# Optimization experiments

Hardware: AMD Instinct MI355X
Metric: run time of the kernel (lower is better)

The kernel has to match this reference:

```python
import jax, jax.numpy as jnp
import numpy as np

B, IN = 8192, 8000
C, S, O = 16, 500, 64          # num_chunks, chunk_size, fc_repr_dim
F = C * O                       # fc_0_out_feat = 1024
E, D, T = 8, 512, 2            # num_experts, fc_task_dim, num_tasks
NC = (32, 2)                    # num_classes per task
EPS = 1e-5


def _bn(h, g, b, axis):
    # training-mode BatchNorm1d: biased variance over the batch axis
    m = h.mean(axis=axis, keepdims=True)
    v = h.var(axis=axis, keepdims=True)
    return (h - m) * jax.lax.rsqrt(v + EPS) * g + b


def _swish(x):
    return x * jax.nn.sigmoid(x)


def setup_inputs() -> dict:
    key = jax.random.key(0)
    ks = jax.random.split(key, 10)
    s = 0.02
    return {
        "x": jax.random.normal(ks[0], (B, IN), dtype=jnp.float32),
        "w0": jax.random.normal(ks[1], (C, O, S), dtype=jnp.float32) * s,
        "b0": jnp.zeros((F,), jnp.float32),
        "bn0_g": jnp.ones((F,), jnp.float32),
        "bn0_b": jnp.zeros((F,), jnp.float32),
        "gate_w": jax.random.normal(ks[2], (T, F, E), dtype=jnp.float32) * s,
        "gate_b": jnp.zeros((T, E), jnp.float32),
        "exp_w": jax.random.normal(ks[3], (E, F, D), dtype=jnp.float32) * s,
        "exp_bn_g": jnp.ones((E, D), jnp.float32),
        "exp_bn_b": jnp.zeros((E, D), jnp.float32),
        "task_w": jax.random.normal(ks[4], (T, D, D), dtype=jnp.float32) * s,
        "task_bn_g": jnp.ones((T, D), jnp.float32),
        "task_bn_b": jnp.zeros((T, D), jnp.float32),
        "fin_w_a": jax.random.normal(ks[5], (D, NC[0]), dtype=jnp.float32) * s,
        "fin_b_a": jnp.zeros((NC[0],), jnp.float32),
        "fin_w_b": jax.random.normal(ks[6], (D, NC[1]), dtype=jnp.float32) * s,
        "fin_b_b": jnp.zeros((NC[1],), jnp.float32),
    }


def reference(x, w0, b0, bn0_g, bn0_b, gate_w, gate_b, exp_w, exp_bn_g,
              exp_bn_b, task_w, task_bn_g, task_bn_b, fin_w_a, fin_b_a,
              fin_w_b, fin_b_b):
    b = x.shape[0]
    # SplitLinear: block-diagonal linear over C chunks of size S -> O each
    h0 = jnp.einsum('bcs,cos->bco', x.reshape(b, C, S), w0).reshape(b, F) + b0
    h0 = _swish(_bn(h0, bn0_g, bn0_b, axis=0))                  # [B, F]
    # per-task gates with softmax over experts
    gates = jax.nn.softmax(
        jnp.einsum('bf,tfe->tbe', h0, gate_w) + gate_b[:, None, :], axis=-1)
    # expert branches: Linear(no bias) + BN + Swish, vectorized over experts
    eh = jnp.einsum('bf,efd->bed', h0, exp_w)                   # [B, E, D]
    eh = _swish(_bn(eh, exp_bn_g, exp_bn_b, axis=0))
    # gate-weighted sum over experts, per task
    mix = jnp.einsum('tbe,bed->tbd', gates, eh)                 # [T, B, D]
    # task branches: Linear(no bias) + BN + Swish
    th = jnp.einsum('tbd,tdk->tbk', mix, task_w)
    th = _swish(_bn(th, task_bn_g[:, None, :], task_bn_b[:, None, :], axis=1))
    out_a = th[0] @ fin_w_a + fin_b_a                           # [B, 32]
    out_b = th[1] @ fin_w_b + fin_b_b                           # [B, 2]
    return jnp.concatenate([out_a, out_b], axis=1)             # [B, 34]
```

## Files before the change

kernel.cpp:

```cpp
#include <hip/hip_runtime.h>
#include <math.h>

#define B_ 8192
#define IN_ 8000
#define C_ 16
#define S_ 500
#define O_ 64
#define F_ 1024
#define E_ 8
#define D_ 512
#define T_ 2
#define OUTW 34
#define EPS_ 1e-5f

typedef __attribute__((ext_vector_type(8))) short bf16x8;
typedef __attribute__((ext_vector_type(4))) float f32x4;

__device__ __forceinline__ float swishf(float x) {
    return x / (1.0f + __expf(-x));
}

__device__ __forceinline__ unsigned short f2bf(float f) {
    union { float f; unsigned u; } c;
    c.f = f;
    unsigned r = c.u + 0x7fffu + ((c.u >> 16) & 1u);
    return (unsigned short)(r >> 16);
}
__device__ __forceinline__ float bf2f(unsigned short b) {
    union { unsigned u; float f; } c;
    c.u = ((unsigned)b) << 16;
    return c.f;
}

__device__ __forceinline__ void gld16(const void* g, void* l) {
    __builtin_amdgcn_global_load_lds(
        (const __attribute__((address_space(1))) void*)g,
        (__attribute__((address_space(3))) void*)l, 16, 0, 0);
}

__global__ __launch_bounds__(256) void k_split(const float* __restrict__ x,
                                               const float* __restrict__ w0,
                                               const float* __restrict__ b0,
                                               unsigned short* __restrict__ h0raw,
                                               float* __restrict__ psum,
                                               float* __restrict__ psq) {
    __shared__ __align__(16) unsigned short As[128 * 72];
    __shared__ __align__(16) unsigned short Bs[64 * 72];
    int tid = threadIdx.x;
    int c = blockIdx.y;
    int brow0 = blockIdx.x * 128;
    const float* xp = x + (size_t)brow0 * IN_ + c * S_;
    const float* wp = w0 + (size_t)c * O_ * S_;

    int w = tid >> 6, lane = tid & 63;
    int l15 = lane & 15, quad = lane >> 4;
    int wm = w * 32;

    f32x4 acc[2][4] = {};

    for (int k0 = 0; k0 < 512; k0 += 64) {
#pragma unroll
        for (int i = 0; i < 8; i++) {
            int li = tid + i * 256;
            int row = li >> 4, c4 = li & 15;
            int gk = k0 + c4 * 4;
            float4 v = make_float4(0.f, 0.f, 0.f, 0.f);
            if (gk + 3 < S_) v = *(const float4*)(xp + (size_t)row * IN_ + gk);
            unsigned short u[4] = { f2bf(v.x), f2bf(v.y), f2bf(v.z), f2bf(v.w) };
            *(ushort4*)&As[row * 72 + c4 * 4] = *(ushort4*)u;
        }
#pragma unroll
        for (int i = 0; i < 4; i++) {
            int li = tid + i * 256;
            int row = li >> 4, c4 = li & 15;
            int gk = k0 + c4 * 4;
            float4 v = make_float4(0.f, 0.f, 0.f, 0.f);
            if (gk + 3 < S_) v = *(const float4*)(wp + (size_t)row * S_ + gk);
            unsigned short u[4] = { f2bf(v.x), f2bf(v.y), f2bf(v.z), f2bf(v.w) };
            *(ushort4*)&Bs[row * 72 + c4 * 4] = *(ushort4*)u;
        }
        __syncthreads();
#pragma unroll
        for (int kk = 0; kk < 64; kk += 32) {
            bf16x8 af[2], wf[4];
#pragma unroll
            for (int i = 0; i < 2; i++)
                af[i] = *(const bf16x8*)&As[(wm + i * 16 + l15) * 72 + kk + quad * 8];
#pragma unroll
            for (int j = 0; j < 4; j++)
                wf[j] = *(const bf16x8*)&Bs[(j * 16 + l15) * 72 + kk + quad * 8];
#pragma unroll
            for (int i = 0; i < 2; i++)
#pragma unroll
                for (int j = 0; j < 4; j++)
                    acc[i][j] = __builtin_amdgcn_mfma_f32_16x16x32_bf16(af[i], wf[j], acc[i][j], 0, 0, 0);
        }
        __syncthreads();
    }

    int colbase = c * O_;
    float sj[4], qj[4];
#pragma unroll
    for (int j = 0; j < 4; j++) {
        int col = j * 16 + l15;
        float bb = b0[colbase + col];
        float s = 0.f, q = 0.f;
#pragma unroll
        for (int i = 0; i < 2; i++) {
#pragma unroll
            for (int reg = 0; reg < 4; reg++) {
                float v = acc[i][j][reg] + bb;
                int rl = wm + i * 16 + quad * 4 + reg;
                h0raw[(size_t)(brow0 + rl) * F_ + colbase + col] = f2bf(v);
                s += v; q += v * v;
            }
        }
        s += __shfl_down(s, 32, 64); s += __shfl_down(s, 16, 64);
        q += __shfl_down(q, 32, 64); q += __shfl_down(q, 16, 64);
        sj[j] = s; qj[j] = q;
    }
    __syncthreads();
    float* red = (float*)As;
    if (lane < 16) {
#pragma unroll
        for (int j = 0; j < 4; j++) {
            int col = j * 16 + l15;
            red[col * 4 + w] = sj[j];
            red[256 + col * 4 + w] = qj[j];
        }
    }
    __syncthreads();
    if (tid < 64) {
        float ss = red[tid * 4] + red[tid * 4 + 1] + red[tid * 4 + 2] + red[tid * 4 + 3];
        float qq = red[256 + tid * 4] + red[256 + tid * 4 + 1] + red[256 + tid * 4 + 2] + red[256 + tid * 4 + 3];
        size_t idx = (size_t)blockIdx.x * F_ + colbase + tid;
        psum[idx] = ss; psq[idx] = qq;
    }
}

__global__ __launch_bounds__(64) void k_stats_b(const float* __restrict__ psum,
                                                const float* __restrict__ psq,
                                                int N, int YS,
                                                const float* __restrict__ g,
                                                const float* __restrict__ beta,
                                                unsigned long long gslab,
                                                float* __restrict__ scale,
                                                float* __restrict__ shift,
                                                unsigned long long oslab) {
    int n = blockIdx.x * 64 + threadIdx.x;
    int z = blockIdx.z;
    float s = 0.f, q = 0.f;
    for (int y = 0; y < YS; y++) {
        size_t idx = ((size_t)(z * YS + y)) * N + n;
        s += psum[idx]; q += psq[idx];
    }
    float mean = s * (1.0f / B_);
    float var = q * (1.0f / B_) - mean * mean;
    float sc = g[z * gslab + n] * rsqrtf(var + EPS_);
    scale[z * oslab + n] = sc;
    shift[z * oslab + n] = beta[z * gslab + n] - mean * sc;
}

__global__ __launch_bounds__(256) void k_wt(const float* __restrict__ in,
                                            unsigned short* __restrict__ out,
                                            int K, int N) {
    __shared__ float t[32][33];
    int k0 = blockIdx.x * 32, n0 = blockIdx.y * 32, z = blockIdx.z;
    const float* ip = in + (size_t)z * K * N;
    unsigned short* op = out + (size_t)z * N * K;
    int tn = threadIdx.x & 31, tk = threadIdx.x >> 5;
#pragma unroll
    for (int p = 0; p < 4; p++) {
        int k = tk + p * 8;
        t[k][tn] = ip[(size_t)(k0 + k) * N + n0 + tn];
    }
    __syncthreads();
    int tk2 = threadIdx.x & 31, tn2 = threadIdx.x >> 5;
#pragma unroll
    for (int p = 0; p < 4; p++) {
        int n = tn2 + p * 8;
        op[(size_t)(n0 + n) * K + k0 + tk2] = f2bf(t[tk2][n]);
    }
}

__global__ __launch_bounds__(256) void k_bnswish_gates(const unsigned short* __restrict__ h0,
                                                       const float* __restrict__ scale,
                                                       const float* __restrict__ shift,
                                                       const float* __restrict__ gate_w,
                                                       const float* __restrict__ gate_b,
                                                       unsigned short* __restrict__ h0bf,
                                                       float* __restrict__ gates) {
    int b = blockIdx.x, tid = threadIdx.x;
    float part[16];
#pragma unroll
    for (int i = 0; i < 16; i++) part[i] = 0.f;
    const unsigned short* row = h0 + (size_t)b * F_;
    unsigned short* ob = h0bf + (size_t)b * F_;
    int f0 = tid * 4;
    ushort4 u = *(const ushort4*)(row + f0);
    float4 sc4 = *(const float4*)(scale + f0);
    float4 sh4 = *(const float4*)(shift + f0);
    unsigned short uu[4] = { u.x, u.y, u.z, u.w };
    float scv[4] = { sc4.x, sc4.y, sc4.z, sc4.w };
    float shv[4] = { sh4.x, sh4.y, sh4.z, sh4.w };
    unsigned short ov[4];
#pragma unroll
    for (int j = 0; j < 4; j++) {
        float sw = swishf(scv[j] * bf2f(uu[j]) + shv[j]);
        ov[j] = f2bf(sw);
        const float* gw0 = gate_w + (size_t)(f0 + j) * E_;
        const float* gw1 = gw0 + (size_t)F_ * E_;
#pragma unroll
        for (int e = 0; e < E_; e++) part[e] += sw * gw0[e];
#pragma unroll
        for (int e = 0; e < E_; e++) part[8 + e] += sw * gw1[e];
    }
    *(ushort4*)(ob + f0) = *(ushort4*)ov;
#pragma unroll
    for (int i = 0; i < 16; i++) {
        float v = part[i];
        for (int off = 32; off > 0; off >>= 1) v += __shfl_down(v, off, 64);
        part[i] = v;
    }
    __shared__ float red[4][16];
    __shared__ float gfin[16];
    int wave = tid >> 6, lane = tid & 63;
    if (lane == 0) {
#pragma unroll
        for (int i = 0; i < 16; i++) red[wave][i] = part[i];
    }
    __syncthreads();
    if (tid < 16) {
        float v = red[0][tid] + red[1][tid] + red[2][tid] + red[3][tid];
        int t = tid >> 3, e = tid & 7;
        gfin[tid] = v + gate_b[t * E_ + e];
    }
    __syncthreads();
    if (tid < 2) {
        float mx = -1e30f;
#pragma unroll
        for (int e = 0; e < 8; e++) mx = fmaxf(mx, gfin[tid * 8 + e]);
        float ex[8], sum = 0.f;
#pragma unroll
        for (int e = 0; e < 8; e++) { ex[e] = __expf(gfin[tid * 8 + e] - mx); sum += ex[e]; }
        float inv = 1.0f / sum;
#pragma unroll
        for (int e = 0; e < 8; e++)
            gates[(size_t)tid * (B_ * E_) + (size_t)b * E_ + e] = ex[e] * inv;
    }
}

__global__ __launch_bounds__(256) void k_gemm_bf16(const unsigned short* __restrict__ A,
                                                   unsigned long long aslab,
                                                   const unsigned short* __restrict__ Wt,
                                                   unsigned long long wslab,
                                                   unsigned short* __restrict__ C,
                                                   unsigned long long cslab, int K,
                                                   float* __restrict__ psum,
                                                   float* __restrict__ psq) {
    __shared__ __align__(16) unsigned short As[128 * 32];
    __shared__ __align__(16) unsigned short Ws[128 * 32];
    int z = blockIdx.z;
    A  += (size_t)z * aslab;
    Wt += (size_t)z * wslab;
    C  += (size_t)z * cslab;
    const int N = gridDim.y * 128;
    int row0 = blockIdx.x * 128, col0 = blockIdx.y * 128;
    int tid = threadIdx.x;
    int w = tid >> 6, lane = tid & 63;
    int l15 = lane & 15, quad = lane >> 4;

    const unsigned short* ga0 = A  + (size_t)(row0 + w * 32 + (lane >> 2)) * K + (lane & 3) * 8;
    const unsigned short* ga1 = ga0 + 16 * (size_t)K;
    const unsigned short* gw0 = Wt + (size_t)(col0 + w * 32 + (lane >> 2)) * K + (lane & 3) * 8;
    const unsigned short* gw1 = gw0 + 16 * (size_t)K;
    unsigned short* la0 = As + (w * 32) * 32;
    unsigned short* la1 = As + (w * 32 + 16) * 32;
    unsigned short* lw0 = Ws + (w * 32) * 32;
    unsigned short* lw1 = Ws + (w * 32 + 16) * 32;

    int wm = (w & 1) * 64, wn = (w >> 1) * 64;
    const unsigned short* Afr = As + (size_t)(wm + l15) * 32 + quad * 8;
    const unsigned short* Wfr = Ws + (size_t)(wn + l15) * 32 + quad * 8;

    f32x4 acc[4][4] = {};

    for (int k0 = 0; k0 < K; k0 += 32) {
        gld16(ga0 + k0, la0);
        gld16(ga1 + k0, la1);
        gld16(gw0 + k0, lw0);
        gld16(gw1 + k0, lw1);
        __syncthreads();
        bf16x8 af[4], wf[4];
#pragma unroll
        for (int i = 0; i < 4; i++) af[i] = *(const bf16x8*)(Afr + i * 16 * 32);
#pragma unroll
        for (int j = 0; j < 4; j++) wf[j] = *(const bf16x8*)(Wfr + j * 16 * 32);
#pragma unroll
        for (int i = 0; i < 4; i++)
#pragma unroll
            for (int j = 0; j < 4; j++)
                acc[i][j] = __builtin_amdgcn_mfma_f32_16x16x32_bf16(af[i], wf[j], acc[i][j], 0, 0, 0);
        __syncthreads();
    }

#pragma unroll
    for (int i = 0; i < 4; i++) {
        int r = row0 + wm + i * 16 + quad * 4;
#pragma unroll
        for (int j = 0; j < 4; j++) {
            int cc = col0 + wn + j * 16 + l15;
            unsigned short* cp = C + (size_t)r * N + cc;
#pragma unroll
            for (int reg = 0; reg < 4; reg++)
                cp[(size_t)reg * N] = f2bf(acc[i][j][reg]);
        }
    }

    float* red = (float*)As;
    float sj[4], qj[4];
#pragma unroll
    for (int j = 0; j < 4; j++) {
        float s = 0.f, q = 0.f;
#pragma unroll
        for (int i = 0; i < 4; i++)
#pragma unroll
            for (int reg = 0; reg < 4; reg++) {
                float v = acc[i][j][reg];
                s += v; q += v * v;
            }
        s += __shfl_down(s, 32, 64); s += __shfl_down(s, 16, 64);
        q += __shfl_down(q, 32, 64); q += __shfl_down(q, 16, 64);
        sj[j] = s; qj[j] = q;
    }
    if (lane < 16) {
#pragma unroll
        for (int j = 0; j < 4; j++) {
            int cib = wn + j * 16 + lane;
            red[cib * 2 + (w & 1)] = sj[j];
            red[256 + cib * 2 + (w & 1)] = qj[j];
        }
    }
    __syncthreads();
    if (tid < 128) {
        float s = red[tid * 2] + red[tid * 2 + 1];
        float q = red[256 + tid * 2] + red[256 + tid * 2 + 1];
        size_t row = (size_t)z * gridDim.x + blockIdx.x;
        psum[row * N + col0 + tid] = s;
        psq[row * N + col0 + tid] = q;
    }
}

__global__ __launch_bounds__(512, 2) void k_gemm256(const unsigned short* __restrict__ A,
                                                    const unsigned short* __restrict__ Wt,
                                                    unsigned short* __restrict__ Cc,
                                                    int N, int K,
                                                    float* __restrict__ psum,
                                                    float* __restrict__ psq) {
    __shared__ __align__(16) unsigned short lds[2][2][2][8192];
    int tid = threadIdx.x;
    int w = tid >> 6, lane = tid & 63;
    int l15 = lane & 15, quad = lane >> 4;
    int wm = w >> 2, wn = w & 3;

    int lin = blockIdx.y * gridDim.x + blockIdx.x;
    int cpx = (gridDim.x * gridDim.y) >> 3;
    int swz = (lin & 7) * cpx + (lin >> 3);
    int bx = swz & (gridDim.x - 1), by = swz / gridDim.x;
    int row0 = bx * 256, col0 = by * 256;

    int srow = tid >> 3, sperm = (tid & 7) ^ (srow & 7);
    const unsigned short* pA = A  + (size_t)(row0 + srow) * K + sperm * 8;
    const unsigned short* pB = Wt + (size_t)(col0 + srow) * K + sperm * 8;

    int aoffs[2];
#pragma unroll
    for (int kk = 0; kk < 2; kk++)
        aoffs[kk] = l15 * 64 + ((kk * 4 + quad) ^ (l15 & 7)) * 8;

    f32x4 acc[8][4] = {};
    bf16x8 afr[4][2], bfr[2][2];
    int nt = K >> 6;

#define STAGE256(t1, nb) do {                                                              \
    const unsigned short* sA = pA + (size_t)(t1) * 64;                                     \
    const unsigned short* sB = pB + (size_t)(t1) * 64;                                     \
    _Pragma("unroll")                                                                      \
    for (int h = 0; h < 2; h++)                                                            \
        _Pragma("unroll")                                                                  \
        for (int L = 0; L < 2; L++) {                                                      \
            gld16(sA + (size_t)(h * 128 + L * 64) * K, &lds[nb][0][h][w * 512 + L * 4096]);\
            gld16(sB + (size_t)(h * 128 + L * 64) * K, &lds[nb][1][h][w * 512 + L * 4096]);\
        }                                                                                  \
} while (0)

#define LDA256(mh) do {                                                                    \
    _Pragma("unroll")                                                                      \
    for (int mf = 0; mf < 4; mf++)                                                         \
        _Pragma("unroll")                                                                  \
        for (int kk = 0; kk < 2; kk++)                                                     \
            afr[mf][kk] = *(const bf16x8*)(Ab + ((mh) * 4 + mf) * 1024 + aoffs[kk]);       \
} while (0)

#define LDB256(nh) do {                                                                    \
    _Pragma("unroll")                                                                      \
    for (int nf = 0; nf < 2; nf++)                                                         \
        _Pragma("unroll")                                                                  \
        for (int kk = 0; kk < 2; kk++)                                                     \
            bfr[nf][kk] = *(const bf16x8*)(Bb + ((nh) * 2 + nf) * 1024 + aoffs[kk]);       \
} while (0)

#define MMA256(mh, nh) do {                                                                \
    _Pragma("unroll")                                                                      \
    for (int mf = 0; mf < 4; mf++)                                                         \
        _Pragma("unroll")                                                                  \
        for (int nf = 0; nf < 2; nf++)                                                     \
            _Pragma("unroll")                                                              \
            for (int kk = 0; kk < 2; kk++)                                                 \
                acc[(mh) * 4 + mf][(nh) * 2 + nf] = __builtin_amdgcn_mfma_f32_16x16x32_bf16(\
                    afr[mf][kk], bfr[nf][kk], acc[(mh) * 4 + mf][(nh) * 2 + nf], 0, 0, 0); \
} while (0)

#define PHASE_MID()                                                                        \
    __builtin_amdgcn_s_barrier();                                                          \
    asm volatile("s_waitcnt lgkmcnt(0)" ::: "memory");                                     \
    __builtin_amdgcn_sched_barrier(0);                                                     \
    __builtin_amdgcn_s_setprio(1);

#define PHASE_END()                                                                        \
    __builtin_amdgcn_s_setprio(0);                                                         \
    __builtin_amdgcn_sched_barrier(0);                                                     \
    __builtin_amdgcn_s_barrier();

    STAGE256(0, 0);
    asm volatile("s_waitcnt vmcnt(0)" ::: "memory");
    __builtin_amdgcn_s_barrier();

    for (int t = 0; t < nt; t++) {
        int buf = t & 1;
        const unsigned short* Ab = &lds[buf][0][wm][0];
        const unsigned short* Bb = &lds[buf][1][wn >> 1][(wn & 1) * 4096];
        LDA256(0); LDB256(0);
        if (t + 1 < nt) STAGE256(t + 1, buf ^ 1);
        PHASE_MID();
        MMA256(0, 0);
        PHASE_END();
        LDB256(1);
        PHASE_MID();
        MMA256(0, 1);
        PHASE_END();
        LDA256(1);
        PHASE_MID();
        MMA256(1, 1);
        PHASE_END();
        LDB256(0);
        PHASE_MID();
        MMA256(1, 0);
        __builtin_amdgcn_s_setprio(0);
        __builtin_amdgcn_sched_barrier(0);
        asm volatile("s_waitcnt vmcnt(0)" ::: "memory");
        __builtin_amdgcn_s_barrier();
    }
#undef STAGE256
#undef LDA256
#undef LDB256
#undef MMA256
#undef PHASE_MID
#undef PHASE_END

    __syncthreads();

#pragma unroll
    for (int mf = 0; mf < 8; mf++) {
        int r = row0 + wm * 128 + mf * 16 + quad * 4;
#pragma unroll
        for (int nf = 0; nf < 4; nf++) {
            int cc = col0 + wn * 64 + nf * 16 + l15;
            unsigned short* cp = Cc + (size_t)r * N + cc;
#pragma unroll
            for (int reg = 0; reg < 4; reg++)
                cp[(size_t)reg * N] = f2bf(acc[mf][nf][reg]);
        }
    }

    float* red = (float*)&lds[0][0][0][0];
    float* redq = red + 512;
    float sj[4], qj[4];
#pragma unroll
    for (int nf = 0; nf < 4; nf++) {
        float s = 0.f, q = 0.f;
#pragma unroll
        for (int mf = 0; mf < 8; mf++)
#pragma unroll
            for (int reg = 0; reg < 4; reg++) {
                float v = acc[mf][nf][reg];
                s += v; q += v * v;
            }
        s += __shfl_down(s, 32, 64); s += __shfl_down(s, 16, 64);
        q += __shfl_down(q, 32, 64); q += __shfl_down(q, 16, 64);
        sj[nf] = s; qj[nf] = q;
    }
    if (quad == 0) {
#pragma unroll
        for (int nf = 0; nf < 4; nf++) {
            int cib = wn * 64 + nf * 16 + l15;
            red[cib * 2 + wm] = sj[nf];
            redq[cib * 2 + wm] = qj[nf];
        }
    }
    __syncthreads();
    if (tid < 256) {
        float s = red[tid * 2] + red[tid * 2 + 1];
        float q = redq[tid * 2] + redq[tid * 2 + 1];
        psum[(size_t)bx * N + col0 + tid] = s;
        psq [(size_t)bx * N + col0 + tid] = q;
    }
}

__global__ __launch_bounds__(256) void k_mix(const unsigned short* __restrict__ eh,
                                             const float* __restrict__ scale,
                                             const float* __restrict__ shift,
                                             const float* __restrict__ gates,
                                             unsigned short* __restrict__ mix) {
    __shared__ float scl[E_ * D_], shl[E_ * D_];
    __shared__ float gl[2][2][8];
    int tid = threadIdx.x;
#pragma unroll
    for (int i = 0; i < 4; i++) {
        int li = tid + i * 256;
        ((float4*)scl)[li] = ((const float4*)scale)[li];
        ((float4*)shl)[li] = ((const float4*)shift)[li];
    }
    if (tid < 32) {
        int sub = tid >> 4, t = (tid >> 3) & 1, e = tid & 7;
        gl[sub][t][e] = gates[(size_t)t * (B_ * E_) + (size_t)(blockIdx.x * 2 + sub) * E_ + e];
    }
    __syncthreads();
    int sub = tid >> 7;
    int b = blockIdx.x * 2 + sub;
    int d0 = (tid & 127) * 4;
    float a0[4] = {0.f, 0.f, 0.f, 0.f}, a1[4] = {0.f, 0.f, 0.f, 0.f};
#pragma unroll
    for (int e = 0; e < E_; e++) {
        ushort4 u = *(const ushort4*)&eh[(size_t)b * (E_ * D_) + e * D_ + d0];
        float4 sc4 = *(const float4*)&scl[e * D_ + d0];
        float4 sh4 = *(const float4*)&shl[e * D_ + d0];
        float g0 = gl[sub][0][e], g1 = gl[sub][1][e];
        unsigned short uu[4] = { u.x, u.y, u.z, u.w };
        float scv[4] = { sc4.x, sc4.y, sc4.z, sc4.w };
        float shv[4] = { sh4.x, sh4.y, sh4.z, sh4.w };
#pragma unroll
        for (int l = 0; l < 4; l++) {
            float sw = swishf(scv[l] * bf2f(uu[l]) + shv[l]);
            a0[l] += g0 * sw;
            a1[l] += g1 * sw;
        }
    }
    unsigned short o0[4], o1[4];
#pragma unroll
    for (int l = 0; l < 4; l++) { o0[l] = f2bf(a0[l]); o1[l] = f2bf(a1[l]); }
    *(ushort4*)&mix[(size_t)b * D_ + d0] = *(ushort4*)o0;
    *(ushort4*)&mix[(size_t)(B_ * D_) + (size_t)b * D_ + d0] = *(ushort4*)o1;
}

__global__ __launch_bounds__(256) void k_final(const unsigned short* __restrict__ th,
                                               const float* __restrict__ scale,
                                               const float* __restrict__ shift,
                                               const float* __restrict__ fwa,
                                               const float* __restrict__ fba,
                                               const float* __restrict__ fwb,
                                               const float* __restrict__ fbb,
                                               float* __restrict__ out) {
    __shared__ float t0[8][D_], t1[8][D_];
    __shared__ float pb[64];
    int tid = threadIdx.x;
    int b0 = blockIdx.x * 8;
#pragma unroll
    for (int t = 0; t < 2; t++) {
#pragma unroll
        for (int i = 0; i < 4; i++) {
            int li = tid + i * 256;
            int row = li >> 7, d = (li & 127) * 4;
            ushort4 u = *(const ushort4*)&th[((size_t)t * B_ + b0 + row) * D_ + d];
            unsigned short uu[4] = { u.x, u.y, u.z, u.w };
            float* dst = t ? &t1[row][d] : &t0[row][d];
#pragma unroll
            for (int l = 0; l < 4; l++)
                dst[l] = swishf(scale[t * D_ + d + l] * bf2f(uu[l]) + shift[t * D_ + d + l]);
        }
    }
    __syncthreads();
    {
        int row = tid >> 5, col = tid & 31;
        float acc = fba[col];
        for (int d = 0; d < D_; d++) acc += t0[row][d] * fwa[d * 32 + col];
        out[(size_t)(b0 + row) * OUTW + col] = acc;
    }
    if (tid < 64) {
        int row = tid >> 3, colb = (tid >> 2) & 1, part = tid & 3;
        float a = 0.f;
        for (int d = part * 128; d < part * 128 + 128; d++) a += t1[row][d] * fwb[d * 2 + colb];
        pb[tid] = a;
    }
    __syncthreads();
    if (tid < 16) {
        int row = tid >> 1, colb = tid & 1;
        int base = row * 8 + colb * 4;
        float a = fbb[colb] + pb[base] + pb[base + 1] + pb[base + 2] + pb[base + 3];
        out[(size_t)(b0 + row) * OUTW + 32 + colb] = a;
    }
}

extern "C" void kernel_launch(void* const* d_in, const int* in_sizes, int n_in,
                              void* d_out, int out_size, void* d_ws, size_t ws_size,
                              hipStream_t stream) {
    const float* x        = (const float*)d_in[0];
    const float* w0       = (const float*)d_in[1];
    const float* b0       = (const float*)d_in[2];
    const float* bn0_g    = (const float*)d_in[3];
    const float* bn0_b    = (const float*)d_in[4];
    const float* gate_w   = (const float*)d_in[5];
    const float* gate_b   = (const float*)d_in[6];
    const float* exp_w    = (const float*)d_in[7];
    const float* exp_bn_g = (const float*)d_in[8];
    const float* exp_bn_b = (const float*)d_in[9];
    const float* task_w   = (const float*)d_in[10];
    const float* task_bn_g= (const float*)d_in[11];
    const float* task_bn_b= (const float*)d_in[12];
    const float* fwa      = (const float*)d_in[13];
    const float* fba      = (const float*)d_in[14];
    const float* fwb      = (const float*)d_in[15];
    const float* fbb      = (const float*)d_in[16];
    float* out = (float*)d_out;

    float* ws = (float*)d_ws;
    unsigned short* ehbf  = (unsigned short*)ws;
    unsigned short* h0raw = (unsigned short*)(ws + 16777216);
    unsigned short* thbf  = ehbf;
    unsigned short* mixbf = h0raw;
    unsigned short* h0bf  = (unsigned short*)(ws + 20971520);
    unsigned short* wtE   = (unsigned short*)(ws + 25165824);
    unsigned short* twt   = (unsigned short*)(ws + 27262976);
    float* gates = ws + 27525120;
    float* sc0   = ws + 27656192;
    float* sh0   = sc0 + 1024;
    float* scE   = sh0 + 1024;
    float* shE   = scE + 4096;
    float* scT   = shE + 4096;
    float* shT   = scT + 1024;
    float* psum  = shT + 1024;
    float* psq   = psum + 262144;

    k_wt<<<dim3(32, 16, 8), 256, 0, stream>>>(exp_w, wtE, F_, D_);
    k_wt<<<dim3(16, 16, 2), 256, 0, stream>>>(task_w, twt, D_, D_);
    k_split<<<dim3(64, 16), 256, 0, stream>>>(x, w0, b0, h0raw, psum, psq);
    k_stats_b<<<dim3(16, 1, 1), 64, 0, stream>>>(psum, psq, F_, 64, bn0_g, bn0_b, 0ull, sc0, sh0, 0ull);
    k_bnswish_gates<<<dim3(B_), 256, 0, stream>>>(h0raw, sc0, sh0, gate_w, gate_b, h0bf, gates);
    k_gemm256<<<dim3(32, 16), 512, 0, stream>>>(h0bf, wtE, ehbf, E_ * D_, F_, psum, psq);
    k_stats_b<<<dim3(64, 1, 1), 64, 0, stream>>>(psum, psq, E_ * D_, 32, exp_bn_g, exp_bn_b, 0ull, scE, shE, 0ull);
    k_mix<<<dim3(B_ / 2), 256, 0, stream>>>(ehbf, scE, shE, gates, mixbf);
    k_gemm_bf16<<<dim3(64, 4, 2), 256, 0, stream>>>(mixbf, (unsigned long long)(B_ * D_),
                                                    twt, (unsigned long long)(D_ * D_),
                                                    thbf, (unsigned long long)(B_ * D_), D_,
                                                    psum, psq);
    k_stats_b<<<dim3(8, 1, 2), 64, 0, stream>>>(psum, psq, D_, 64, task_bn_g, task_bn_b, 512ull, scT, shT, 512ull);
    k_final<<<dim3(B_ / 8), 256, 0, stream>>>(thbf, scT, shT, fwa, fba, fwb, fbb, out);
}
```

Measured before the change: 687.9 us.

## Split BN-swish from gate computation and compute gates with bf16 MFMA

The fused per-row BN/swish plus gate kernel is split into a lightweight elementwise BN-swish kernel that handles 4 rows per block, and a separate gate kernel. The gate kernel stages the transposed gate weights in LDS as bf16 and computes the gate logits with 16x16x32 bf16 MFMA, doing the softmax via lane shuffles. The aim is to replace 8192 blocks of scalar FMA, 16 wave reductions and two barriers each with matrix-core work. The final head also splits its accumulation across several partial sums to get more ILP. This adds one kernel launch and one extra read of h0bf, and the gate logits now use bf16 weights.

```diff
diff --git a/kernel.cpp b/kernel.cpp
--- a/kernel.cpp
+++ b/kernel.cpp
@@ -183,70 +183,75 @@
     }
 }
 
-__global__ __launch_bounds__(256) void k_bnswish_gates(const unsigned short* __restrict__ h0,
-                                                       const float* __restrict__ scale,
-                                                       const float* __restrict__ shift,
-                                                       const float* __restrict__ gate_w,
-                                                       const float* __restrict__ gate_b,
-                                                       unsigned short* __restrict__ h0bf,
-                                                       float* __restrict__ gates) {
-    int b = blockIdx.x, tid = threadIdx.x;
-    float part[16];
-#pragma unroll
-    for (int i = 0; i < 16; i++) part[i] = 0.f;
-    const unsigned short* row = h0 + (size_t)b * F_;
-    unsigned short* ob = h0bf + (size_t)b * F_;
+__global__ __launch_bounds__(256) void k_bnswish(const unsigned short* __restrict__ h0,
+                                                 const float* __restrict__ scale,
+                                                 const float* __restrict__ shift,
+                                                 unsigned short* __restrict__ h0bf) {
+    int tid = threadIdx.x;
     int f0 = tid * 4;
-    ushort4 u = *(const ushort4*)(row + f0);
     float4 sc4 = *(const float4*)(scale + f0);
     float4 sh4 = *(const float4*)(shift + f0);
-    unsigned short uu[4] = { u.x, u.y, u.z, u.w };
     float scv[4] = { sc4.x, sc4.y, sc4.z, sc4.w };
     float shv[4] = { sh4.x, sh4.y, sh4.z, sh4.w };
-    unsigned short ov[4];
-#pragma unroll
-    for (int j = 0; j < 4; j++) {
-        float sw = swishf(scv[j] * bf2f(uu[j]) + shv[j]);
-        ov[j] = f2bf(sw);
-        const float* gw0 = gate_w + (size_t)(f0 + j) * E_;
-        const float* gw1 = gw0 + (size_t)F_ * E_;
-#pragma unroll
-        for (int e = 0; e < E_; e++) part[e] += sw * gw0[e];
-#pragma unroll
-        for (int e = 0; e < E_; e++) part[8 + e] += sw * gw1[e];
-    }
-    *(ushort4*)(ob + f0) = *(ushort4*)ov;
-#pragma unroll
-    for (int i = 0; i < 16; i++) {
-        float v = part[i];
-        for (int off = 32; off > 0; off >>= 1) v += __shfl_down(v, off, 64);
-        part[i] = v;
-    }
-    __shared__ float red[4][16];
-    __shared__ float gfin[16];
-    int wave = tid >> 6, lane = tid & 63;
-    if (lane == 0) {
-#pragma unroll
-        for (int i = 0; i < 16; i++) red[wave][i] = part[i];
-    }
-    __syncthreads();
-    if (tid < 16) {
-        float v = red[0][tid] + red[1][tid] + red[2][tid] + red[3][tid];
-        int t = tid >> 3, e = tid & 7;
-        gfin[tid] = v + gate_b[t * E_ + e];
-    }
-    __syncthreads();
-    if (tid < 2) {
-        float mx = -1e30f;
-#pragma unroll
-        for (int e = 0; e < 8; e++) mx = fmaxf(mx, gfin[tid * 8 + e]);
-        float ex[8], sum = 0.f;
-#pragma unroll
-        for (int e = 0; e < 8; e++) { ex[e] = __expf(gfin[tid * 8 + e] - mx); sum += ex[e]; }
-        float inv = 1.0f / sum;
-#pragma unroll
-        for (int e = 0; e < 8; e++)
-            gates[(size_t)tid * (B_ * E_) + (size_t)b * E_ + e] = ex[e] * inv;
+    size_t base = (size_t)blockIdx.x * 4 * F_ + f0;
+#pragma unroll
+    for (int r = 0; r < 4; r++) {
+        ushort4 u = *(const ushort4*)(h0 + base + (size_t)r * F_);
+        unsigned short uu[4] = { u.x, u.y, u.z, u.w };
+        unsigned short ov[4];
+#pragma unroll
+        for (int j = 0; j < 4; j++)
+            ov[j] = f2bf(swishf(scv[j] * bf2f(uu[j]) + shv[j]));
+        *(ushort4*)(h0bf + base + (size_t)r * F_) = *(ushort4*)ov;
+    }
+}
+
+__global__ __launch_bounds__(256) void k_gates(const unsigned short* __restrict__ h0bf,
+                                               const float* __restrict__ gate_w,
+                                               const float* __restrict__ gate_b,
+                                               float* __restrict__ gates) {
+    __shared__ __align__(16) unsigned short gwt[16 * 1032];
+    int tid = threadIdx.x;
+    for (int idx = tid; idx < 16 * 1024; idx += 256) {
+        int col = idx >> 10, f = idx & 1023;
+        int t = col >> 3, e = col & 7;
+        gwt[col * 1032 + f] = f2bf(gate_w[(size_t)t * (F_ * E_) + (size_t)f * E_ + e]);
+    }
+    __syncthreads();
+    int w = tid >> 6, lane = tid & 63;
+    int l15 = lane & 15, quad = lane >> 4;
+    int r0 = blockIdx.x * 128 + w * 32;
+    f32x4 acc[2] = {};
+    const unsigned short* a0p = h0bf + (size_t)(r0 + l15) * F_ + quad * 8;
+    const unsigned short* a1p = a0p + (size_t)16 * F_;
+    const unsigned short* wp = &gwt[l15 * 1032 + quad * 8];
+#pragma unroll 4
+    for (int k0 = 0; k0 < F_; k0 += 32) {
+        bf16x8 wf  = *(const bf16x8*)(wp + k0);
+        bf16x8 af0 = *(const bf16x8*)(a0p + k0);
+        bf16x8 af1 = *(const bf16x8*)(a1p + k0);
+        acc[0] = __builtin_amdgcn_mfma_f32_16x16x32_bf16(af0, wf, acc[0], 0, 0, 0);
+        acc[1] = __builtin_amdgcn_mfma_f32_16x16x32_bf16(af1, wf, acc[1], 0, 0, 0);
+    }
+    float gb = gate_b[l15];
+    int t = l15 >> 3, e = l15 & 7;
+#pragma unroll
+    for (int i = 0; i < 2; i++) {
+#pragma unroll
+        for (int reg = 0; reg < 4; reg++) {
+            float v = acc[i][reg] + gb;
+            float m = v;
+            m = fmaxf(m, __shfl_xor(m, 1, 64));
+            m = fmaxf(m, __shfl_xor(m, 2, 64));
+            m = fmaxf(m, __shfl_xor(m, 4, 64));
+            float ex = __expf(v - m);
+            float s = ex;
+            s += __shfl_xor(s, 1, 64);
+            s += __shfl_xor(s, 2, 64);
+            s += __shfl_xor(s, 4, 64);
+            int row = r0 + i * 16 + quad * 4 + reg;
+            gates[(size_t)t * (B_ * E_) + (size_t)row * E_ + e] = ex / s;
+        }
     }
 }
 
@@ -592,14 +597,22 @@
     __syncthreads();
     {
         int row = tid >> 5, col = tid & 31;
-        float acc = fba[col];
-        for (int d = 0; d < D_; d++) acc += t0[row][d] * fwa[d * 32 + col];
-        out[(size_t)(b0 + row) * OUTW + col] = acc;
+        float a0 = 0.f, a1 = 0.f, a2 = 0.f, a3 = 0.f;
+        for (int d = 0; d < D_; d += 4) {
+            a0 += t0[row][d + 0] * fwa[(d + 0) * 32 + col];
+            a1 += t0[row][d + 1] * fwa[(d + 1) * 32 + col];
+            a2 += t0[row][d + 2] * fwa[(d + 2) * 32 + col];
+            a3 += t0[row][d + 3] * fwa[(d + 3) * 32 + col];
+        }
+        out[(size_t)(b0 + row) * OUTW + col] = fba[col] + ((a0 + a1) + (a2 + a3));
     }
     if (tid < 64) {
         int row = tid >> 3, colb = (tid >> 2) & 1, part = tid & 3;
         float a = 0.f;
-        for (int d = part * 128; d < part * 128 + 128; d++) a += t1[row][d] * fwb[d * 2 + colb];
+        for (int d = part * 128; d < part * 128 + 128; d += 2) {
+            a += t1[row][d] * fwb[d * 2 + colb];
+            a += t1[row][d + 1] * fwb[(d + 1) * 2 + colb];
+        }
         pb[tid] = a;
     }
     __syncthreads();
@@ -655,7 +668,8 @@
     k_wt<<<dim3(16, 16, 2), 256, 0, stream>>>(task_w, twt, D_, D_);
     k_split<<<dim3(64, 16), 256, 0, stream>>>(x, w0, b0, h0raw, psum, psq);
     k_stats_b<<<dim3(16, 1, 1), 64, 0, stream>>>(psum, psq, F_, 64, bn0_g, bn0_b, 0ull, sc0, sh0, 0ull);
-    k_bnswish_gates<<<dim3(B_), 256, 0, stream>>>(h0raw, sc0, sh0, gate_w, gate_b, h0bf, gates);
+    k_bnswish<<<dim3(B_ / 4), 256, 0, stream>>>(h0raw, sc0, sh0, h0bf);
+    k_gates<<<dim3(B_ / 128), 256, 0, stream>>>(h0bf, gate_w, gate_b, gates);
     k_gemm256<<<dim3(32, 16), 512, 0, stream>>>(h0bf, wtE, ehbf, E_ * D_, F_, psum, psq);
     k_stats_b<<<dim3(64, 1, 1), 64, 0, stream>>>(psum, psq, E_ * D_, 32, exp_bn_g, exp_bn_b, 0ull, scE, shE, 0ull);
     k_mix<<<dim3(B_ / 2), 256, 0, stream>>>(ehbf, scE, shE, gates, mixbf);
```

New measurement: 648.2 us. -5.8%, faster.

## Compute gate logits with MFMA over 32-row tiles and merge weight transposes

Applied to the files above, without the earlier changes.

The per-row BN+swish+gate kernel (one block per batch row, scalar FMAs over fp32 gate weights) is replaced by a kernel that handles 32 rows per block. It stages the bf16 activations and a bf16 copy of the gate weights in shared memory and computes the 16 gate logits with bf16 MFMA, then applies softmax. The two weight-transpose launches are also merged into one grid. This cuts per-row launch and reduction overhead and uses matrix cores, at the cost of bf16 gate weights (lower precision) and re-converting gate_w into shared memory in every block.

```diff
diff --git a/kernel.cpp b/kernel.cpp
--- a/kernel.cpp
+++ b/kernel.cpp
@@ -161,13 +161,25 @@
     shift[z * oslab + n] = beta[z * gslab + n] - mean * sc;
 }
 
-__global__ __launch_bounds__(256) void k_wt(const float* __restrict__ in,
-                                            unsigned short* __restrict__ out,
-                                            int K, int N) {
+__global__ __launch_bounds__(256) void k_wt2(const float* __restrict__ exp_w,
+                                             unsigned short* __restrict__ wtE,
+                                             const float* __restrict__ task_w,
+                                             unsigned short* __restrict__ twt) {
+    int z = blockIdx.z;
+    const float* ip; unsigned short* op; int K, N;
+    if (z < 8) {
+        K = F_; N = D_;
+        ip = exp_w + (size_t)z * K * N;
+        op = wtE + (size_t)z * N * K;
+    } else {
+        if (blockIdx.x >= 16) return;
+        K = D_; N = D_;
+        int zz = z - 8;
+        ip = task_w + (size_t)zz * K * N;
+        op = twt + (size_t)zz * N * K;
+    }
     __shared__ float t[32][33];
-    int k0 = blockIdx.x * 32, n0 = blockIdx.y * 32, z = blockIdx.z;
-    const float* ip = in + (size_t)z * K * N;
-    unsigned short* op = out + (size_t)z * N * K;
+    int k0 = blockIdx.x * 32, n0 = blockIdx.y * 32;
     int tn = threadIdx.x & 31, tk = threadIdx.x >> 5;
 #pragma unroll
     for (int p = 0; p < 4; p++) {
@@ -183,70 +195,77 @@
     }
 }
 
-__global__ __launch_bounds__(256) void k_bnswish_gates(const unsigned short* __restrict__ h0,
-                                                       const float* __restrict__ scale,
-                                                       const float* __restrict__ shift,
-                                                       const float* __restrict__ gate_w,
-                                                       const float* __restrict__ gate_b,
-                                                       unsigned short* __restrict__ h0bf,
-                                                       float* __restrict__ gates) {
-    int b = blockIdx.x, tid = threadIdx.x;
-    float part[16];
-#pragma unroll
-    for (int i = 0; i < 16; i++) part[i] = 0.f;
-    const unsigned short* row = h0 + (size_t)b * F_;
-    unsigned short* ob = h0bf + (size_t)b * F_;
-    int f0 = tid * 4;
-    ushort4 u = *(const ushort4*)(row + f0);
+__global__ __launch_bounds__(512) void k_bng(const unsigned short* __restrict__ h0,
+                                             const float* __restrict__ scale,
+                                             const float* __restrict__ shift,
+                                             const float* __restrict__ gate_w,
+                                             const float* __restrict__ gate_b,
+                                             unsigned short* __restrict__ h0bf,
+                                             float* __restrict__ gates) {
+    __shared__ __align__(16) unsigned short gwt[16 * 1032];
+    __shared__ __align__(16) unsigned short As[32 * 1032];
+    __shared__ float plog[4][32][16];
+    int tid = threadIdx.x;
+    int brow = blockIdx.x * 32;
+    for (int idx = tid; idx < 16 * 1024; idx += 512) {
+        int col = idx >> 10, f = idx & 1023;
+        int t = col >> 3, e = col & 7;
+        gwt[col * 1032 + f] = f2bf(gate_w[(size_t)t * (F_ * E_) + (size_t)f * E_ + e]);
+    }
+    int f0 = (tid & 255) * 4;
+    int rh = tid >> 8;
     float4 sc4 = *(const float4*)(scale + f0);
     float4 sh4 = *(const float4*)(shift + f0);
-    unsigned short uu[4] = { u.x, u.y, u.z, u.w };
     float scv[4] = { sc4.x, sc4.y, sc4.z, sc4.w };
     float shv[4] = { sh4.x, sh4.y, sh4.z, sh4.w };
-    unsigned short ov[4];
-#pragma unroll
-    for (int j = 0; j < 4; j++) {
-        float sw = swishf(scv[j] * bf2f(uu[j]) + shv[j]);
-        ov[j] = f2bf(sw);
-        const float* gw0 = gate_w + (size_t)(f0 + j) * E_;
-        const float* gw1 = gw0 + (size_t)F_ * E_;
-#pragma unroll
-        for (int e = 0; e < E_; e++) part[e] += sw * gw0[e];
-#pragma unroll
-        for (int e = 0; e < E_; e++) part[8 + e] += sw * gw1[e];
-    }
-    *(ushort4*)(ob + f0) = *(ushort4*)ov;
-#pragma unroll
-    for (int i = 0; i < 16; i++) {
-        float v = part[i];
-        for (int off = 32; off > 0; off >>= 1) v += __shfl_down(v, off, 64);
-        part[i] = v;
-    }
-    __shared__ float red[4][16];
-    __shared__ float gfin[16];
-    int wave = tid >> 6, lane = tid & 63;
-    if (lane == 0) {
-#pragma unroll
-        for (int i = 0; i < 16; i++) red[wave][i] = part[i];
-    }
-    __syncthreads();
-    if (tid < 16) {
-        float v = red[0][tid] + red[1][tid] + red[2][tid] + red[3][tid];
-        int t = tid >> 3, e = tid & 7;
-        gfin[tid] = v + gate_b[t * E_ + e];
-    }
-    __syncthreads();
-    if (tid < 2) {
-        float mx = -1e30f;
-#pragma unroll
-        for (int e = 0; e < 8; e++) mx = fmaxf(mx, gfin[tid * 8 + e]);
-        float ex[8], sum = 0.f;
-#pragma unroll
-        for (int e = 0; e < 8; e++) { ex[e] = __expf(gfin[tid * 8 + e] - mx); sum += ex[e]; }
-        float inv = 1.0f / sum;
-#pragma unroll
-        for (int e = 0; e < 8; e++)
-            gates[(size_t)tid * (B_ * E_) + (size_t)b * E_ + e] = ex[e] * inv;
+#pragma unroll
+    for (int r = 0; r < 16; r++) {
+        int row = rh * 16 + r;
+        ushort4 u = *(const ushort4*)(h0 + (size_t)(brow + row) * F_ + f0);
+        unsigned short uu[4] = { u.x, u.y, u.z, u.w };
+        unsigned short ov[4];
+#pragma unroll
+        for (int j = 0; j < 4; j++)
+            ov[j] = f2bf(swishf(scv[j] * bf2f(uu[j]) + shv[j]));
+        *(ushort4*)(h0bf + (size_t)(brow + row) * F_ + f0) = *(ushort4*)ov;
+        *(ushort4*)&As[row * 1032 + f0] = *(ushort4*)ov;
+    }
+    __syncthreads();
+    int w = tid >> 6, lane = tid & 63;
+    int l15 = lane & 15, quad = lane >> 4;
+    int slot = w & 1, kq = w >> 1;
+    f32x4 acc = {};
+    const unsigned short* ap = &As[(slot * 16 + l15) * 1032 + kq * 256 + quad * 8];
+    const unsigned short* wp = &gwt[l15 * 1032 + kq * 256 + quad * 8];
+#pragma unroll
+    for (int k0 = 0; k0 < 256; k0 += 32) {
+        bf16x8 af = *(const bf16x8*)(ap + k0);
+        bf16x8 wf = *(const bf16x8*)(wp + k0);
+        acc = __builtin_amdgcn_mfma_f32_16x16x32_bf16(af, wf, acc, 0, 0, 0);
+    }
+#pragma unroll
+    for (int reg = 0; reg < 4; reg++)
+        plog[kq][slot * 16 + quad * 4 + reg][l15] = acc[reg];
+    __syncthreads();
+    if (tid < 32) {
+        int r = tid;
+        float lg[16];
+#pragma unroll
+        for (int c = 0; c < 16; c++)
+            lg[c] = plog[0][r][c] + plog[1][r][c] + plog[2][r][c] + plog[3][r][c] + gate_b[c];
+#pragma unroll
+        for (int t = 0; t < 2; t++) {
+            float mx = -1e30f;
+#pragma unroll
+            for (int e = 0; e < 8; e++) mx = fmaxf(mx, lg[t * 8 + e]);
+            float ex[8], s = 0.f;
+#pragma unroll
+            for (int e = 0; e < 8; e++) { ex[e] = __expf(lg[t * 8 + e] - mx); s += ex[e]; }
+            float inv = 1.0f / s;
+#pragma unroll
+            for (int e = 0; e < 8; e++)
+                gates[(size_t)t * (B_ * E_) + (size_t)(brow + r) * E_ + e] = ex[e] * inv;
+        }
     }
 }
 
@@ -651,11 +670,10 @@
     float* psum  = shT + 1024;
     float* psq   = psum + 262144;
 
-    k_wt<<<dim3(32, 16, 8), 256, 0, stream>>>(exp_w, wtE, F_, D_);
-    k_wt<<<dim3(16, 16, 2), 256, 0, stream>>>(task_w, twt, D_, D_);
+    k_wt2<<<dim3(32, 16, 10), 256, 0, stream>>>(exp_w, wtE, task_w, twt);
     k_split<<<dim3(64, 16), 256, 0, stream>>>(x, w0, b0, h0raw, psum, psq);
     k_stats_b<<<dim3(16, 1, 1), 64, 0, stream>>>(psum, psq, F_, 64, bn0_g, bn0_b, 0ull, sc0, sh0, 0ull);
-    k_bnswish_gates<<<dim3(B_), 256, 0, stream>>>(h0raw, sc0, sh0, gate_w, gate_b, h0bf, gates);
+    k_bng<<<dim3(256), 512, 0, stream>>>(h0raw, sc0, sh0, gate_w, gate_b, h0bf, gates);
     k_gemm256<<<dim3(32, 16), 512, 0, stream>>>(h0bf, wtE, ehbf, E_ * D_, F_, psum, psq);
     k_stats_b<<<dim3(64, 1, 1), 64, 0, stream>>>(psum, psq, E_ * D_, 32, exp_bn_g, exp_bn_b, 0ull, scE, shE, 0ull);
     k_mix<<<dim3(B_ / 2), 256, 0, stream>>>(ehbf, scE, shE, gates, mixbf);
```

Result: faster. 638.7 us (-7.2%).
